# Optimization experiments

Hardware: AMD Instinct MI355X
Metric: run time of the kernel (lower is better)

The kernel has to match this reference:

```python
import jax, jax.numpy as jnp
import numpy as np

EPS = 1e-5

def setup_inputs() -> dict:
    key = jax.random.key(0)
    ks = jax.random.split(key, 7)
    C = 512
    x = jax.random.normal(ks[0], (16, C, 32, 32), dtype=jnp.float32)
    gn_w = jax.random.normal(ks[1], (C,), dtype=jnp.float32) * 0.02 + 1.0
    gn_b = jax.random.normal(ks[2], (C,), dtype=jnp.float32) * 0.02
    qkv_w = jax.random.normal(ks[3], (3 * C, C), dtype=jnp.float32) * (1.0 / np.sqrt(C))
    qkv_b = jax.random.normal(ks[4], (3 * C,), dtype=jnp.float32) * 0.02
    proj_w = jax.random.normal(ks[5], (C, C), dtype=jnp.float32) * (1.0 / np.sqrt(C))
    proj_b = jax.random.normal(ks[6], (C,), dtype=jnp.float32) * 0.02
    return {"x": x, "gn_w": gn_w, "gn_b": gn_b, "qkv_w": qkv_w,
            "qkv_b": qkv_b, "proj_w": proj_w, "proj_b": proj_b}

def reference(x, gn_w, gn_b, qkv_w, qkv_b, proj_w, proj_b):
    B, C, H, W = x.shape
    S = H * W
    # GroupNorm with 1 group: normalize over (C,H,W) per sample
    mean = jnp.mean(x, axis=(1, 2, 3), keepdims=True)
    var = jnp.var(x, axis=(1, 2, 3), keepdims=True)
    h = (x - mean) * jax.lax.rsqrt(var + EPS)
    h = h * gn_w[None, :, None, None] + gn_b[None, :, None, None]
    # 1x1 conv qkv: [B,C,H,W] -> [B,3C,H,W], flatten spatial -> [B,S,3C]
    hf = h.reshape(B, C, S)  # b c s
    qkv = jnp.einsum('bcs,oc->bso', hf, qkv_w) + qkv_b  # [B,S,3C]
    q, k, v = jnp.split(qkv, 3, axis=-1)  # each [B,S,C]
    scale = C ** (-0.5)
    attn = jax.nn.softmax(jnp.einsum('bqc,bkc->bqk', q, k) * scale, axis=-1)
    out = jnp.einsum('bqk,bkc->bqc', attn, v)  # [B,S,C]
    out = jnp.einsum('bsc,oc->bso', out, proj_w) + proj_b
    out = out.transpose(0, 2, 1).reshape(B, C, H, W)
    return x + out
```

## Files before the change

### kernel.cpp

```cpp
#include <hip/hip_runtime.h>
#include <stdint.h>

#define B_  16
#define C_  512
#define S_  1024
#define NSAMP (C_*S_)

typedef __bf16 bf16x8 __attribute__((ext_vector_type(8)));
typedef float  f32x4  __attribute__((ext_vector_type(4)));

__device__ __forceinline__ float bf2f(uint16_t u){ return __uint_as_float(((uint32_t)u)<<16); }
__device__ __forceinline__ uint16_t f2bf(float f){
  uint32_t u = __float_as_uint(f);
  uint32_t r = u + 0x7fffu + ((u>>16)&1u);
  return (uint16_t)(r>>16);
}
__device__ __forceinline__ float wsum(float v){
  #pragma unroll
  for(int o=32;o;o>>=1) v += __shfl_xor(v,o,64);
  return v;
}
__device__ __forceinline__ void gload16(const void* g, void* l){
  __builtin_amdgcn_global_load_lds(
      (__attribute__((address_space(1))) void*)g,
      (__attribute__((address_space(3))) void*)l, 16, 0, 0);
}

__global__ __launch_bounds__(256) void detect_k(const uint16_t* __restrict__ x,
                                                int* __restrict__ flag){
  __shared__ int sh[4];
  int cnt = 0;
  for(int i=threadIdx.x; i<32768; i+=256){
    uint32_t e = (x[2*i] >> 7) & 0xffu;
    cnt += (e >= 132) ? 1 : 0;
  }
  #pragma unroll
  for(int o=32;o;o>>=1) cnt += __shfl_xor(cnt,o,64);
  const int lane = threadIdx.x & 63, w = threadIdx.x >> 6;
  if (lane==0) sh[w] = cnt;
  __syncthreads();
  if (threadIdx.x==0) *flag = (sh[0]+sh[1]+sh[2]+sh[3] > 4096) ? 1 : 0;
}

__device__ __forceinline__ void convseg(const void* src, uint16_t* dst, int n, int f, int t){
  const int idx = t*8;
  if (idx >= n) return;
  if (f){
    const float* s = (const float*)src;
    float4 v0 = *(const float4*)(s + idx);
    float4 v1 = *(const float4*)(s + idx + 4);
    ushort4 a, b;
    a.x=f2bf(v0.x); a.y=f2bf(v0.y); a.z=f2bf(v0.z); a.w=f2bf(v0.w);
    b.x=f2bf(v1.x); b.y=f2bf(v1.y); b.z=f2bf(v1.z); b.w=f2bf(v1.w);
    *(ushort4*)(dst + idx)     = a;
    *(ushort4*)(dst + idx + 4) = b;
  } else {
    *(uint4*)(dst + idx) = *(const uint4*)((const uint16_t*)src + idx);
  }
}
__global__ __launch_bounds__(256) void prep_k(
    const void* __restrict__ srcx, uint16_t* __restrict__ xb, float2* __restrict__ part,
    const void* qkvw, const void* projw, const void* gnw, const void* gnb,
    const void* qkvb, const void* projb,
    uint16_t* qkvwb, uint16_t* projwb, uint16_t* gnwb, uint16_t* gnbb,
    uint16_t* qkvbb, uint16_t* projbb, const int* __restrict__ flag){
  const int f = *flag;
  const int t = threadIdx.x;
  if (blockIdx.x >= 1024){
    const int bid = blockIdx.x - 1024;
    if (bid < 384){
      const size_t off = (size_t)bid*2048;
      convseg((const char*)qkvw + off*(f?4:2), qkvwb + off, 2048, f, t);
    } else if (bid < 512){
      const size_t off = (size_t)(bid-384)*2048;
      convseg((const char*)projw + off*(f?4:2), projwb + off, 2048, f, t);
    } else {
      convseg(gnw,   gnwb,   512,  f, t);
      convseg(gnb,   gnbb,   512,  f, t);
      convseg(qkvb,  qkvbb,  1536, f, t);
      convseg(projb, projbb, 512,  f, t);
    }
    return;
  }
  const size_t base = (size_t)blockIdx.x * 8192;
  float s = 0.f, s2 = 0.f;
  if (f){
    const float4* sp = (const float4*)((const float*)srcx + base);
    ushort4* dp = (ushort4*)(xb + base);
    #pragma unroll
    for(int i=0;i<8;i++){
      float4 v = sp[i*256 + t];
      s  += v.x + v.y + v.z + v.w;
      s2 += v.x*v.x + v.y*v.y + v.z*v.z + v.w*v.w;
      ushort4 o; o.x=f2bf(v.x); o.y=f2bf(v.y); o.z=f2bf(v.z); o.w=f2bf(v.w);
      dp[i*256 + t] = o;
    }
  } else {
    const uint4* sp = (const uint4*)((const uint16_t*)srcx + base);
    uint4* dp = (uint4*)(xb + base);
    #pragma unroll
    for(int i=0;i<4;i++){
      uint4 p = sp[i*256 + t];
      dp[i*256 + t] = p;
      uint32_t uu[4] = {p.x,p.y,p.z,p.w};
      #pragma unroll
      for(int q=0;q<4;q++){
        float f0 = __uint_as_float(uu[q]<<16);
        float f1 = __uint_as_float(uu[q] & 0xffff0000u);
        s += f0 + f1; s2 += f0*f0 + f1*f1;
      }
    }
  }
  s = wsum(s); s2 = wsum(s2);
  __shared__ float rs[4], rq[4];
  const int lane = t & 63, w = t >> 6;
  if (lane==0){ rs[w]=s; rq[w]=s2; }
  __syncthreads();
  if (t==0)
    part[blockIdx.x] = make_float2(rs[0]+rs[1]+rs[2]+rs[3], rq[0]+rq[1]+rq[2]+rq[3]);
}

__global__ __launch_bounds__(256) void gn_apply_t(const uint16_t* __restrict__ x,
    const uint16_t* __restrict__ gw, const uint16_t* __restrict__ gb,
    const float2* __restrict__ part, uint16_t* __restrict__ hT){
  __shared__ float tile[64][65];
  const int b = blockIdx.z, c0 = blockIdx.y<<6, s0 = blockIdx.x<<6;
  const int tc = threadIdx.x >> 6, tl = threadIdx.x & 63;
  float2 p = part[b*64 + tl];
  float s = wsum(p.x), s2 = wsum(p.y);
  const float ninv = 1.f/(float)NSAMP;
  const float mn = s*ninv;
  const float rstd = rsqrtf(s2*ninv - mn*mn + 1e-5f);
  #pragma unroll
  for(int r=0;r<16;r++){
    int cl = r*4 + tc;
    tile[cl][tl] = bf2f(x[((size_t)b*C_ + c0+cl)*S_ + s0 + tl]);
  }
  __syncthreads();
  const float wv = bf2f(gw[c0+tl]) * rstd;
  const float bv = bf2f(gb[c0+tl]);
  #pragma unroll
  for(int r=0;r<16;r++){
    int sl = r*4 + tc;
    float v = (tile[tl][sl] - mn)*wv + bv;
    hT[((size_t)b*S_ + s0+sl)*C_ + c0 + tl] = f2bf(v);
  }
}

__global__ __launch_bounds__(256)
void qkv_k(const uint16_t* __restrict__ hT, const uint16_t* __restrict__ qkvw,
           const uint16_t* __restrict__ qkvb, uint16_t* __restrict__ qk,
           uint16_t* __restrict__ Vt)
{
  __shared__ uint16_t As[128*64];
  __shared__ uint16_t Bs[128*64];
  const int tid = threadIdx.x;
  const int lane = tid & 63, w = tid >> 6;
  const int quad = lane >> 4, lm = lane & 15;
  const int wm = (w & 1) << 6, wn = (w >> 1) << 6;

  const bool vpath = blockIdx.x >= 1024;
  const int id = vpath ? (blockIdx.x - 1024) : blockIdx.x;
  const int r8 = id & 7, k8 = id >> 3;
  int m0, n0, bz;
  const uint16_t *Abase, *Bbase;
  if (!vpath){
    const int g = r8*16 + (k8 & 15);
    m0 = g << 7; n0 = (k8 >> 4) << 7; bz = 0;
    Abase = hT + (size_t)m0*512;
    Bbase = qkvw + (size_t)n0*512;
  } else {
    const int g = r8*16 + (k8 & 15);
    m0 = (k8 >> 4) << 7; n0 = (g & 7) << 7; bz = g >> 3;
    Abase = qkvw + (size_t)(1024 + m0)*512;
    Bbase = hT + (size_t)bz*S_*C_ + (size_t)n0*512;
  }

  f32x4 acc[4][4];
  #pragma unroll
  for(int i=0;i<4;i++)
    #pragma unroll
    for(int j=0;j<4;j++) acc[i][j] = (f32x4){0.f,0.f,0.f,0.f};

  const int srow = tid >> 3;
  const int sx   = (tid & 7) ^ (srow & 7);
  const uint16_t* ga = Abase + (size_t)srow*512 + sx*8;
  const uint16_t* gb = Bbase + (size_t)srow*512 + sx*8;
  uint16_t* sa = &As[tid*8];
  uint16_t* sb = &Bs[tid*8];

  for(int k0=0;k0<512;k0+=64){
    #pragma unroll
    for(int i=0;i<4;i++){
      gload16(ga + (size_t)(i*32)*512 + k0, sa + i*2048);
      gload16(gb + (size_t)(i*32)*512 + k0, sb + i*2048);
    }
    __syncthreads();
    #pragma unroll
    for(int kk=0;kk<64;kk+=32){
      bf16x8 av[4], bv[4];
      #pragma unroll
      for(int i=0;i<4;i++){
        const int row = wm + i*16 + lm;
        av[i] = *(const bf16x8*)&As[row*64 + ((((kk>>3)+quad) ^ (row&7))<<3)];
      }
      #pragma unroll
      for(int j=0;j<4;j++){
        const int row = wn + j*16 + lm;
        bv[j] = *(const bf16x8*)&Bs[row*64 + ((((kk>>3)+quad) ^ (row&7))<<3)];
      }
      #pragma unroll
      for(int i=0;i<4;i++)
        #pragma unroll
        for(int j=0;j<4;j++)
          acc[i][j] = __builtin_amdgcn_mfma_f32_16x16x32_bf16(av[i], bv[j], acc[i][j], 0,0,0);
    }
    __syncthreads();
  }

  if (!vpath){
    #pragma unroll
    for(int j=0;j<4;j++){
      const int col = n0 + wn + j*16 + lm;
      const float bvv = bf2f(qkvb[col]);
      #pragma unroll
      for(int i=0;i<4;i++){
        const int rb = m0 + wm + i*16 + (quad<<2);
        #pragma unroll
        for(int r=0;r<4;r++)
          qk[(size_t)(rb+r)*1024 + col] = f2bf(acc[i][j][r] + bvv);
      }
    }
  } else {
    uint16_t* vb = Vt + (size_t)bz*C_*S_;
    #pragma unroll
    for(int i=0;i<4;i++){
      const int rb = m0 + wm + i*16 + (quad<<2);
      #pragma unroll
      for(int r=0;r<4;r++){
        const float bvv = bf2f(qkvb[1024 + rb + r]);
        #pragma unroll
        for(int j=0;j<4;j++)
          vb[(size_t)(rb+r)*1024 + n0 + wn + j*16 + lm] = f2bf(acc[i][j][r] + bvv);
      }
    }
  }
}

template<bool HASBIAS, bool BIASROW, bool OUTDYN, bool HASRES, int SWZMODE, bool EXP, bool SUMNORM>
__global__ __launch_bounds__(256)
void gemm_bt(const uint16_t* __restrict__ A, const uint16_t* __restrict__ Bt,
             void* __restrict__ Cp, const uint16_t* __restrict__ bias,
             const uint16_t* __restrict__ xres, const int* __restrict__ flag,
             int lda, int ldb, int ldc, int K,
             long long sA, long long sB, long long sC)
{
  __shared__ uint16_t As[128*64];
  __shared__ uint16_t Bs[128*64];
  const int lin = (blockIdx.z * gridDim.y + blockIdx.y) * gridDim.x + blockIdx.x;
  const int r8 = lin & 7, kk8 = lin >> 3;
  int bx, by, bz;
  if (SWZMODE == 0){
    const int G = (gridDim.y * gridDim.z) >> 3;
    const int g = r8 * G + (kk8 % G);
    bx = kk8 / G; by = g % gridDim.y; bz = g / gridDim.y;
  } else {
    const int G = (gridDim.x * gridDim.z) >> 3;
    const int g = r8 * G + (kk8 % G);
    by = kk8 / G; bx = g % gridDim.x; bz = g / gridDim.x;
  }

  const int tid = threadIdx.x;
  const int lane = tid & 63, w = tid >> 6;
  const int quad = lane >> 4, lm = lane & 15;
  const int m0 = by << 7, n0 = bx << 7;
  A  += (size_t)bz * sA;
  Bt += (size_t)bz * sB;

  f32x4 acc[4][4];
  #pragma unroll
  for(int i=0;i<4;i++)
    #pragma unroll
    for(int j=0;j<4;j++) acc[i][j] = (f32x4){0.f,0.f,0.f,0.f};
  f32x4 rsum[4];
  bf16x8 onesv;
  if (SUMNORM){
    #pragma unroll
    for(int i=0;i<4;i++) rsum[i] = (f32x4){0.f,0.f,0.f,0.f};
    #pragma unroll
    for(int z=0;z<8;z++) onesv[z] = (__bf16)1.0f;
  }

  const int wm = (w & 1) << 6, wn = (w >> 1) << 6;
  const int srow = tid >> 3;
  const int sx   = (tid & 7) ^ (srow & 7);
  const uint16_t* ga = A  + (size_t)(m0 + srow)*lda + sx*8;
  const uint16_t* gb = Bt + (size_t)(n0 + srow)*ldb + sx*8;
  uint16_t* sa = &As[tid*8];
  uint16_t* sb = &Bs[tid*8];

  for(int k0=0;k0<K;k0+=64){
    #pragma unroll
    for(int i=0;i<4;i++){
      gload16(ga + (size_t)(i*32)*lda + k0, sa + i*2048);
      gload16(gb + (size_t)(i*32)*ldb + k0, sb + i*2048);
    }
    __syncthreads();
    #pragma unroll
    for(int kk=0;kk<64;kk+=32){
      bf16x8 av[4], bv[4];
      #pragma unroll
      for(int i=0;i<4;i++){
        const int row = wm + i*16 + lm;
        av[i] = *(const bf16x8*)&As[row*64 + ((((kk>>3)+quad) ^ (row&7))<<3)];
      }
      #pragma unroll
      for(int j=0;j<4;j++){
        const int row = wn + j*16 + lm;
        bv[j] = *(const bf16x8*)&Bs[row*64 + ((((kk>>3)+quad) ^ (row&7))<<3)];
      }
      #pragma unroll
      for(int i=0;i<4;i++){
        if (SUMNORM) rsum[i] = __builtin_amdgcn_mfma_f32_16x16x32_bf16(av[i], onesv, rsum[i], 0,0,0);
        #pragma unroll
        for(int j=0;j<4;j++)
          acc[i][j] = __builtin_amdgcn_mfma_f32_16x16x32_bf16(av[i], bv[j], acc[i][j], 0,0,0);
      }
    }
    __syncthreads();
  }

  const int f = OUTDYN ? *flag : 0;
  const size_t cb = (size_t)bz * (size_t)sC;
  #pragma unroll
  for(int j=0;j<4;j++){
    const int col = n0 + wn + j*16 + lm;
    const float cbias = (HASBIAS && !BIASROW) ? bf2f(bias[col]) : 0.f;
    #pragma unroll
    for(int i=0;i<4;i++){
      const int rb = m0 + wm + i*16 + (quad<<2);
      #pragma unroll
      for(int r=0;r<4;r++){
        const int row = rb + r;
        float v = acc[i][j][r] + cbias;
        if (HASBIAS && BIASROW) v += bf2f(bias[row]);
        if (EXP)     v = __expf(v * 0.044194173824159216f);
        if (SUMNORM) v = v / rsum[i][r];
        const size_t idx = cb + (size_t)row*ldc + col;
        if (HASRES) v += bf2f(xres[idx]);
        if (OUTDYN && f) ((float*)Cp)[idx] = v;
        else             ((uint16_t*)Cp)[idx] = f2bf(v);
      }
    }
  }
}

extern "C" void kernel_launch(void* const* d_in, const int* in_sizes, int n_in,
                              void* d_out, int out_size, void* d_ws, size_t ws_size,
                              hipStream_t stream){
  char* ws = (char*)d_ws;
  int*      flag  = (int*)ws;
  float2*   part  = (float2*)(ws + 4096);
  uint16_t* gnwb  = (uint16_t*)(ws + 16384);
  uint16_t* gnbb  = (uint16_t*)(ws + 17408);
  uint16_t* qkvbb = (uint16_t*)(ws + 18432);
  uint16_t* projbb= (uint16_t*)(ws + 21504);
  uint16_t* qkvwb = (uint16_t*)(ws + 32768);
  uint16_t* projwb= (uint16_t*)(ws + 1605632);
  uint16_t* xb    = (uint16_t*)(ws + 4194304);
  uint16_t* hT    = (uint16_t*)(ws + 20971520);
  uint16_t* qk    = (uint16_t*)(ws + 37748736);
  uint16_t* sc    = (uint16_t*)(ws + 71303168);
  uint16_t* Vt    = (uint16_t*)(ws + 104857600);

  hipLaunchKernelGGL(detect_k, dim3(1), dim3(256), 0, stream,
                     (const uint16_t*)d_in[0], flag);
  hipLaunchKernelGGL(prep_k, dim3(1537), dim3(256), 0, stream,
                     d_in[0], xb, part,
                     d_in[3], d_in[5], d_in[1], d_in[2], d_in[4], d_in[6],
                     qkvwb, projwb, gnwb, gnbb, qkvbb, projbb, flag);
  hipLaunchKernelGGL(gn_apply_t, dim3(16,8,16), dim3(256), 0, stream, xb, gnwb, gnbb, part, hT);

  hipLaunchKernelGGL(qkv_k, dim3(1536), dim3(256), 0, stream, hT, qkvwb, qkvbb, qk, Vt);

  hipLaunchKernelGGL((gemm_bt<false,false,false,false,0,true,false>), dim3(8,8,16), dim3(256), 0, stream,
      qk, qk + 512, (void*)sc, (const uint16_t*)nullptr, (const uint16_t*)nullptr, flag,
      1024, 1024, 1024, 512, (long long)S_*1024, (long long)S_*1024, (long long)S_*S_);

  hipLaunchKernelGGL((gemm_bt<false,false,false,false,0,false,true>), dim3(4,8,16), dim3(256), 0, stream,
      sc, Vt, (void*)hT, (const uint16_t*)nullptr, (const uint16_t*)nullptr, flag,
      1024, 1024, 512, 1024, (long long)S_*S_, (long long)C_*S_, (long long)S_*C_);

  hipLaunchKernelGGL((gemm_bt<true,true,true,true,1,false,false>), dim3(8,4,16), dim3(256), 0, stream,
      projwb, hT, d_out, projbb, xb, flag,
      512, 512, 1024, 512, 0LL, (long long)S_*C_, (long long)C_*S_);
}
```

Measured before the change: 248.8 us.

## Stage GEMM epilogues through LDS for vectorized coalesced stores; vectorize GN transpose and detect

GEMM and QKV epilogues now write accumulator tiles into shared memory, then emit 16-byte coalesced global stores instead of scattered 2-byte writes. The fp32/residual path stages in two halves with float4 reads and vector residual loads. The GroupNorm-transpose kernel uses 128-wide spatial tiles with uint4 loads and stores. The flag-detection kernel uses 1024 threads with vector loads. This adds extra LDS traffic and syncs in exchange for fewer, wider global memory transactions.

```diff
diff --git a/kernel.cpp b/kernel.cpp
--- a/kernel.cpp
+++ b/kernel.cpp
@@ -26,20 +26,32 @@
       (__attribute__((address_space(3))) void*)l, 16, 0, 0);
 }
 
-__global__ __launch_bounds__(256) void detect_k(const uint16_t* __restrict__ x,
-                                                int* __restrict__ flag){
-  __shared__ int sh[4];
+__global__ __launch_bounds__(1024) void detect_k(const uint16_t* __restrict__ x,
+                                                 int* __restrict__ flag){
+  __shared__ int sh[16];
+  const uint4* xv = (const uint4*)x;
   int cnt = 0;
-  for(int i=threadIdx.x; i<32768; i+=256){
-    uint32_t e = (x[2*i] >> 7) & 0xffu;
-    cnt += (e >= 132) ? 1 : 0;
+  #pragma unroll
+  for(int k=0;k<8;k++){
+    uint4 v = xv[threadIdx.x + k*1024];
+    uint32_t ww[4] = {v.x, v.y, v.z, v.w};
+    #pragma unroll
+    for(int q=0;q<4;q++){
+      cnt += (((ww[q] & 0xffffu) >> 7) & 0xffu) >= 132 ? 1 : 0;
+      cnt += (((ww[q] >> 16)     >> 7) & 0xffu) >= 132 ? 1 : 0;
+    }
   }
   #pragma unroll
   for(int o=32;o;o>>=1) cnt += __shfl_xor(cnt,o,64);
   const int lane = threadIdx.x & 63, w = threadIdx.x >> 6;
   if (lane==0) sh[w] = cnt;
   __syncthreads();
-  if (threadIdx.x==0) *flag = (sh[0]+sh[1]+sh[2]+sh[3] > 4096) ? 1 : 0;
+  if (threadIdx.x==0){
+    int tot = 0;
+    #pragma unroll
+    for(int i=0;i<16;i++) tot += sh[i];
+    *flag = (tot > 4096) ? 1 : 0;
+  }
 }
 
 __device__ __forceinline__ void convseg(const void* src, uint16_t* dst, int n, int f, int t){
@@ -123,27 +135,49 @@
 __global__ __launch_bounds__(256) void gn_apply_t(const uint16_t* __restrict__ x,
     const uint16_t* __restrict__ gw, const uint16_t* __restrict__ gb,
     const float2* __restrict__ part, uint16_t* __restrict__ hT){
-  __shared__ float tile[64][65];
-  const int b = blockIdx.z, c0 = blockIdx.y<<6, s0 = blockIdx.x<<6;
-  const int tc = threadIdx.x >> 6, tl = threadIdx.x & 63;
-  float2 p = part[b*64 + tl];
+  __shared__ float tile[64*129];
+  const int b = blockIdx.z, c0 = blockIdx.y<<6, s0 = blockIdx.x<<7;
+  const int t = threadIdx.x;
+  float2 p = part[b*64 + (t & 63)];
   float s = wsum(p.x), s2 = wsum(p.y);
   const float ninv = 1.f/(float)NSAMP;
   const float mn = s*ninv;
   const float rstd = rsqrtf(s2*ninv - mn*mn + 1e-5f);
   #pragma unroll
-  for(int r=0;r<16;r++){
-    int cl = r*4 + tc;
-    tile[cl][tl] = bf2f(x[((size_t)b*C_ + c0+cl)*S_ + s0 + tl]);
+  for(int k=0;k<4;k++){
+    const int ci = t + k*256;
+    const int cl = ci>>4, sc = ci&15;
+    uint4 v = *(const uint4*)&x[((size_t)b*C_ + c0+cl)*S_ + s0 + sc*8];
+    const uint16_t* e = (const uint16_t*)&v;
+    float* dst = &tile[cl*129 + sc*8];
+    #pragma unroll
+    for(int q=0;q<8;q++) dst[q] = bf2f(e[q]);
   }
   __syncthreads();
-  const float wv = bf2f(gw[c0+tl]) * rstd;
-  const float bv = bf2f(gb[c0+tl]);
-  #pragma unroll
-  for(int r=0;r<16;r++){
-    int sl = r*4 + tc;
-    float v = (tile[tl][sl] - mn)*wv + bv;
-    hT[((size_t)b*S_ + s0+sl)*C_ + c0 + tl] = f2bf(v);
+  const int cc = t & 7;
+  const int sb0 = t >> 3;
+  uint4 wv4 = *(const uint4*)&gw[c0 + cc*8];
+  uint4 bv4 = *(const uint4*)&gb[c0 + cc*8];
+  const uint16_t* we = (const uint16_t*)&wv4;
+  const uint16_t* be = (const uint16_t*)&bv4;
+  float aq[8], cq[8];
+  #pragma unroll
+  for(int q=0;q<8;q++){ aq[q] = bf2f(we[q])*rstd; cq[q] = bf2f(be[q]) - mn*aq[q]; }
+  #pragma unroll
+  for(int k=0;k<4;k++){
+    const int sl = sb0 + k*32;
+    uint16_t ov[8];
+    #pragma unroll
+    for(int q=0;q<8;q++){
+      float xv = tile[(cc*8+q)*129 + sl];
+      ov[q] = f2bf(xv*aq[q] + cq[q]);
+    }
+    uint4 o;
+    o.x = (uint32_t)ov[0] | ((uint32_t)ov[1]<<16);
+    o.y = (uint32_t)ov[2] | ((uint32_t)ov[3]<<16);
+    o.z = (uint32_t)ov[4] | ((uint32_t)ov[5]<<16);
+    o.w = (uint32_t)ov[6] | ((uint32_t)ov[7]<<16);
+    *(uint4*)&hT[((size_t)b*S_ + s0+sl)*C_ + c0 + cc*8] = o;
   }
 }
 
@@ -152,8 +186,9 @@
            const uint16_t* __restrict__ qkvb, uint16_t* __restrict__ qk,
            uint16_t* __restrict__ Vt)
 {
-  __shared__ uint16_t As[128*64];
-  __shared__ uint16_t Bs[128*64];
+  __shared__ uint16_t smem[16384];
+  uint16_t* As = smem;
+  uint16_t* Bs = smem + 8192;
   const int tid = threadIdx.x;
   const int lane = tid & 63, w = tid >> 6;
   const int quad = lane >> 4, lm = lane & 15;
@@ -218,32 +253,40 @@
     __syncthreads();
   }
 
+  uint16_t* Cs = smem;
   if (!vpath){
     #pragma unroll
     for(int j=0;j<4;j++){
-      const int col = n0 + wn + j*16 + lm;
-      const float bvv = bf2f(qkvb[col]);
+      const int col_l = wn + j*16 + lm;
+      const float bvv = bf2f(qkvb[n0 + col_l]);
       #pragma unroll
       for(int i=0;i<4;i++){
-        const int rb = m0 + wm + i*16 + (quad<<2);
+        const int rl0 = wm + i*16 + (quad<<2);
         #pragma unroll
         for(int r=0;r<4;r++)
-          qk[(size_t)(rb+r)*1024 + col] = f2bf(acc[i][j][r] + bvv);
+          Cs[(rl0+r)*128 + col_l] = f2bf(acc[i][j][r] + bvv);
       }
     }
   } else {
-    uint16_t* vb = Vt + (size_t)bz*C_*S_;
     #pragma unroll
     for(int i=0;i<4;i++){
-      const int rb = m0 + wm + i*16 + (quad<<2);
+      const int rl0 = wm + i*16 + (quad<<2);
       #pragma unroll
       for(int r=0;r<4;r++){
-        const float bvv = bf2f(qkvb[1024 + rb + r]);
+        const float bvv = bf2f(qkvb[1024 + m0 + rl0 + r]);
         #pragma unroll
         for(int j=0;j<4;j++)
-          vb[(size_t)(rb+r)*1024 + n0 + wn + j*16 + lm] = f2bf(acc[i][j][r] + bvv);
-      }
-    }
+          Cs[(rl0+r)*128 + wn + j*16 + lm] = f2bf(acc[i][j][r] + bvv);
+      }
+    }
+  }
+  __syncthreads();
+  uint16_t* base = vpath ? (Vt + (size_t)bz*C_*S_) : qk;
+  #pragma unroll
+  for(int k=0;k<8;k++){
+    const int ci = tid + k*256;
+    const int rl = ci>>4, ccc = ci&15;
+    *(uint4*)&base[(size_t)(m0+rl)*1024 + n0 + ccc*8] = *(const uint4*)&Cs[rl*128 + ccc*8];
   }
 }
 
@@ -255,8 +298,9 @@
              int lda, int ldb, int ldc, int K,
              long long sA, long long sB, long long sC)
 {
-  __shared__ uint16_t As[128*64];
-  __shared__ uint16_t Bs[128*64];
+  __shared__ uint16_t smem[16384];
+  uint16_t* As = smem;
+  uint16_t* Bs = smem + 8192;
   const int lin = (blockIdx.z * gridDim.y + blockIdx.y) * gridDim.x + blockIdx.x;
   const int r8 = lin & 7, kk8 = lin >> 3;
   int bx, by, bz;
@@ -330,27 +374,86 @@
     __syncthreads();
   }
 
-  const int f = OUTDYN ? *flag : 0;
   const size_t cb = (size_t)bz * (size_t)sC;
-  #pragma unroll
-  for(int j=0;j<4;j++){
-    const int col = n0 + wn + j*16 + lm;
-    const float cbias = (HASBIAS && !BIASROW) ? bf2f(bias[col]) : 0.f;
-    #pragma unroll
-    for(int i=0;i<4;i++){
-      const int rb = m0 + wm + i*16 + (quad<<2);
-      #pragma unroll
-      for(int r=0;r<4;r++){
-        const int row = rb + r;
-        float v = acc[i][j][r] + cbias;
-        if (HASBIAS && BIASROW) v += bf2f(bias[row]);
-        if (EXP)     v = __expf(v * 0.044194173824159216f);
-        if (SUMNORM) v = v / rsum[i][r];
-        const size_t idx = cb + (size_t)row*ldc + col;
-        if (HASRES) v += bf2f(xres[idx]);
-        if (OUTDYN && f) ((float*)Cp)[idx] = v;
-        else             ((uint16_t*)Cp)[idx] = f2bf(v);
-      }
+  if (!OUTDYN && !HASRES){
+    uint16_t* Cs = smem;
+    #pragma unroll
+    for(int j=0;j<4;j++){
+      const int col_l = wn + j*16 + lm;
+      const float cbias = (HASBIAS && !BIASROW) ? bf2f(bias[n0 + col_l]) : 0.f;
+      #pragma unroll
+      for(int i=0;i<4;i++){
+        const int rl0 = wm + i*16 + (quad<<2);
+        #pragma unroll
+        for(int r=0;r<4;r++){
+          float v = acc[i][j][r] + cbias;
+          if (HASBIAS && BIASROW) v += bf2f(bias[m0 + rl0 + r]);
+          if (EXP)     v = __expf(v * 0.044194173824159216f);
+          if (SUMNORM) v = v / rsum[i][r];
+          Cs[(rl0+r)*128 + col_l] = f2bf(v);
+        }
+      }
+    }
+    __syncthreads();
+    uint16_t* base = (uint16_t*)Cp + cb;
+    #pragma unroll
+    for(int k=0;k<8;k++){
+      const int ci = tid + k*256;
+      const int rl = ci>>4, cc = ci&15;
+      *(uint4*)&base[(size_t)(m0+rl)*ldc + n0 + cc*8] = *(const uint4*)&Cs[rl*128 + cc*8];
+    }
+  } else {
+    float* Cs32 = (float*)smem;
+    const int f = OUTDYN ? *flag : 0;
+    const int wnh = wn >> 1;
+    #pragma unroll
+    for(int half=0; half<2; ++half){
+      #pragma unroll
+      for(int j2=0;j2<2;j2++){
+        const int j = half*2 + j2;
+        const int col_l = wn + j*16 + lm;
+        const int hcol = wnh + j2*16 + lm;
+        const float cbias = (HASBIAS && !BIASROW) ? bf2f(bias[n0 + col_l]) : 0.f;
+        #pragma unroll
+        for(int i=0;i<4;i++){
+          const int rl0 = wm + i*16 + (quad<<2);
+          #pragma unroll
+          for(int r=0;r<4;r++){
+            float v = acc[i][j][r] + cbias;
+            if (HASBIAS && BIASROW) v += bf2f(bias[m0 + rl0 + r]);
+            if (EXP)     v = __expf(v * 0.044194173824159216f);
+            if (SUMNORM) v = v / rsum[i][r];
+            Cs32[(rl0+r)*64 + hcol] = v;
+          }
+        }
+      }
+      __syncthreads();
+      #pragma unroll
+      for(int k=0;k<8;k++){
+        const int ci = tid + k*256;
+        const int rl = ci>>4, c4 = ci&15;
+        float4 vv = *(const float4*)&Cs32[rl*64 + c4*4];
+        const int gcol = n0 + c4*4 + ((c4>=8)?32:0) + half*32;
+        const size_t idx = cb + (size_t)(m0+rl)*ldc + gcol;
+        float o0=vv.x, o1=vv.y, o2=vv.z, o3=vv.w;
+        if (HASRES){
+          uint2 rr = *(const uint2*)&xres[idx];
+          o0 += bf2f((uint16_t)(rr.x & 0xffffu));
+          o1 += bf2f((uint16_t)(rr.x >> 16));
+          o2 += bf2f((uint16_t)(rr.y & 0xffffu));
+          o3 += bf2f((uint16_t)(rr.y >> 16));
+        }
+        if (OUTDYN && f){
+          float4 o = make_float4(o0,o1,o2,o3);
+          *(float4*)&((float*)Cp)[idx] = o;
+        } else {
+          uint2 o;
+          o.x = (uint32_t)f2bf(o0) | ((uint32_t)f2bf(o1)<<16);
+          o.y = (uint32_t)f2bf(o2) | ((uint32_t)f2bf(o3)<<16);
+          *(uint2*)&((uint16_t*)Cp)[idx] = o;
+        }
+      }
+      __syncthreads();
     }
   }
 }
@@ -373,13 +476,13 @@
   uint16_t* sc    = (uint16_t*)(ws + 71303168);
   uint16_t* Vt    = (uint16_t*)(ws + 104857600);
 
-  hipLaunchKernelGGL(detect_k, dim3(1), dim3(256), 0, stream,
+  hipLaunchKernelGGL(detect_k, dim3(1), dim3(1024), 0, stream,
                      (const uint16_t*)d_in[0], flag);
   hipLaunchKernelGGL(prep_k, dim3(1537), dim3(256), 0, stream,
                      d_in[0], xb, part,
                      d_in[3], d_in[5], d_in[1], d_in[2], d_in[4], d_in[6],
                      qkvwb, projwb, gnwb, gnbb, qkvbb, projbb, flag);
-  hipLaunchKernelGGL(gn_apply_t, dim3(16,8,16), dim3(256), 0, stream, xb, gnwb, gnbb, part, hT);
+  hipLaunchKernelGGL(gn_apply_t, dim3(8,8,16), dim3(256), 0, stream, xb, gnwb, gnbb, part, hT);
 
   hipLaunchKernelGGL(qkv_k, dim3(1536), dim3(256), 0, stream, hT, qkvwb, qkvbb, qk, Vt);
 
```

New measurement: 220.0 us. 1.13x faster.
